# Kernel tuning notes

Measured on AMD Instinct MI355X. Metric: run time of the kernel, lower is better.

Reference implementation:

```python
import jax, jax.numpy as jnp
import numpy as np

T, S, B, H, L = 1024, 4096, 1, 1024, 2


def setup_inputs() -> dict:
    key = jax.random.key(0)
    ks = jax.random.split(key, 16)
    sc = 1.0 / np.sqrt(H)
    r = lambda k, shp: (jax.random.normal(k, shp, jnp.float32) * sc)
    return {
        'input_sequence': jax.random.normal(ks[0], (T, B, H), jnp.float32),
        'encoder_out': jax.random.normal(ks[1], (S, B, H), jnp.float32),
        'hidden_state': jax.random.normal(ks[2], (L, B, H), jnp.float32),
        'cell_state': jax.random.normal(ks[3], (L, B, H), jnp.float32),
        'w_ih0': r(ks[4], (4 * H, H)), 'w_hh0': r(ks[5], (4 * H, H)),
        'b_ih0': r(ks[6], (4 * H,)), 'b_hh0': r(ks[7], (4 * H,)),
        'w_ih1': r(ks[8], (4 * H, H)), 'w_hh1': r(ks[9], (4 * H, H)),
        'b_ih1': r(ks[10], (4 * H,)), 'b_hh1': r(ks[11], (4 * H,)),
        'w_cat': r(ks[12], (H, 2 * H)), 'b_cat': r(ks[13], (H,)),
    }


def _lstm_layer(x, h0, c0, w_ih, w_hh, bias):
    # x: [T, B, I]; precompute input projection once (torch gate order i,f,g,o)
    xg = jnp.einsum('tbi,gi->tbg', x, w_ih) + bias  # [T, B, 4H]

    def step(carry, xg_t):
        h, c = carry
        gates = xg_t + h @ w_hh.T
        i, f, g, o = jnp.split(gates, 4, axis=-1)
        c = jax.nn.sigmoid(f) * c + jax.nn.sigmoid(i) * jnp.tanh(g)
        h = jax.nn.sigmoid(o) * jnp.tanh(c)
        return (h, c), h

    (h, c), ys = jax.lax.scan(step, (h0, c0), xg)
    return ys, h, c  # ys: [T, B, H]


def reference(input_sequence, encoder_out, hidden_state, cell_state,
              w_ih0, w_hh0, b_ih0, b_hh0, w_ih1, w_hh1, b_ih1, b_hh1,
              w_cat, b_cat):
    out0, h1, c1 = _lstm_layer(input_sequence, hidden_state[0], cell_state[0],
                               w_ih0, w_hh0, b_ih0 + b_hh0)
    out1, h2, c2 = _lstm_layer(out0, hidden_state[1], cell_state[1],
                               w_ih1, w_hh1, b_ih1 + b_hh1)
    hN = jnp.stack([h1, h2])  # [L, B, H]
    cN = jnp.stack([c1, c2])

    # Attention ('dot'): scores_i = <enc_i, h_last>, softmax over source dim.
    enc = encoder_out[:, 0, :]        # [S, H] (batch = 1)
    target = h2[0]                     # [H]
    scores = enc @ target              # [S]  (replaces per-step torch.dot loop)
    weights = jax.nn.softmax(scores)   # [S]
    context = jnp.einsum('s,sh->h', weights, enc)  # [H] (replaces mul/reduce loop)

    cat = jnp.concatenate([context, h2[0]])          # [2H]
    attentional_hidden = jnp.tanh(cat @ w_cat.T + b_cat)[None, :]  # [1, H]
    return out1, (hN, cN), attentional_hidden
```

## Files before the change

### kernel.cpp

```cpp
#include <hip/hip_runtime.h>
#include <hip/hip_bf16.h>
#include <math.h>

#define T_STEPS 1024
#define HDIM    1024
#define SDIM    4096

__device__ __forceinline__ float sigmoid_f(float x) {
    return __builtin_amdgcn_rcpf(1.0f + __expf(-x));
}
__device__ __forceinline__ float tanh_f(float x) {
    return 1.0f - 2.0f * __builtin_amdgcn_rcpf(1.0f + __expf(2.0f * x));
}

union H2U { unsigned u; _Float16 h[2]; unsigned short s[2]; };

typedef _Float16 half2v __attribute__((ext_vector_type(2)));

__device__ __forceinline__ float fdot2_(unsigned w, unsigned h, float acc) {
#if __has_builtin(__builtin_amdgcn_fdot2)
    return __builtin_amdgcn_fdot2(__builtin_bit_cast(half2v, w),
                                  __builtin_bit_cast(half2v, h), acc, false);
#else
    const half2v a = __builtin_bit_cast(half2v, w);
    const half2v b = __builtin_bit_cast(half2v, h);
    return acc + (float)a[0] * (float)b[0] + (float)a[1] * (float)b[1];
#endif
}

#define GLOAD16(dst, p) asm volatile("global_load_dwordx4 %0, %1, off" \
                                     : "=v"(dst) : "v"(p))
#define GWAIT() asm volatile("s_waitcnt vmcnt(0)" ::: "memory")

__device__ __forceinline__ unsigned long long lda64(const unsigned long long* p) {
    return __hip_atomic_load(p, __ATOMIC_RELAXED, __HIP_MEMORY_SCOPE_AGENT);
}

__device__ __forceinline__ void poll2(const unsigned long long* p0,
                                      const unsigned long long* p1,
                                      unsigned long long& r0, unsigned long long& r1) {
    unsigned long long c0 = lda64(p0), c1 = lda64(p1);
    for (;;) {
        const unsigned long long n0 = lda64(p0);
        const unsigned long long n1 = lda64(p1);
        const unsigned t = (unsigned)c0 | (unsigned)(c0 >> 32) |
                           (unsigned)c1 | (unsigned)(c1 >> 32);
        if (t < 0xFFFF0000u) break;
        c0 = n0; c1 = n1;
    }
    r0 = c0; r1 = c1;
}

__device__ __forceinline__ unsigned pack_pair(unsigned long long v) {
    return (unsigned)(v & 0xFFFFu) | (((unsigned)(v >> 32) & 0xFFFFu) << 16);
}

__global__ __launch_bounds__(256) void cvt_fp16(
    const float* __restrict__ in, _Float16* __restrict__ o, int n)
{
    const int i = (blockIdx.x * 256 + threadIdx.x) * 8;
    if (i + 7 < n) {
        const float4 a = *(const float4*)(in + i);
        const float4 b = *(const float4*)(in + i + 4);
        H2U p0, p1, p2, p3;
        p0.h[0] = (_Float16)a.x; p0.h[1] = (_Float16)a.y;
        p1.h[0] = (_Float16)a.z; p1.h[1] = (_Float16)a.w;
        p2.h[0] = (_Float16)b.x; p2.h[1] = (_Float16)b.y;
        p3.h[0] = (_Float16)b.z; p3.h[1] = (_Float16)b.w;
        *(uint4*)(o + i) = make_uint4(p0.u, p1.u, p2.u, p3.u);
    }
}

__global__ __launch_bounds__(256) void bias_sum(
    const float* __restrict__ a, const float* __restrict__ b, float* __restrict__ o)
{
    const int i = blockIdx.x * 256 + threadIdx.x;
    o[i] = a[i] + b[i];
}

__global__ __launch_bounds__(256) void gemm_xg_h(
    const float* __restrict__ X, const float* __restrict__ W,
    const float* __restrict__ b1, const float* __restrict__ b2,
    _Float16* __restrict__ C, int M, int N, int K)
{
    __shared__ float As[16][64];
    __shared__ float Bs[16][64];
    const int tid = threadIdx.x;
    const int m0 = blockIdx.y * 64, n0 = blockIdx.x * 64;
    const int tx = tid & 15, ty = tid >> 4;
    const int lr = tid >> 2, ls = (tid & 3) << 2;
    float acc[4][4] = {};

    for (int kt = 0; kt < K; kt += 16) {
        const float4 xa = *(const float4*)(X + (size_t)(m0 + lr) * K + kt + ls);
        const float4 wb = *(const float4*)(W + (size_t)(n0 + lr) * K + kt + ls);
        __syncthreads();
        As[ls + 0][lr] = xa.x; As[ls + 1][lr] = xa.y; As[ls + 2][lr] = xa.z; As[ls + 3][lr] = xa.w;
        Bs[ls + 0][lr] = wb.x; Bs[ls + 1][lr] = wb.y; Bs[ls + 2][lr] = wb.z; Bs[ls + 3][lr] = wb.w;
        __syncthreads();
#pragma unroll
        for (int k = 0; k < 16; ++k) {
            const float4 a = *(const float4*)&As[k][ty << 2];
            const float4 b = *(const float4*)&Bs[k][tx << 2];
            acc[0][0] += a.x * b.x; acc[0][1] += a.x * b.y; acc[0][2] += a.x * b.z; acc[0][3] += a.x * b.w;
            acc[1][0] += a.y * b.x; acc[1][1] += a.y * b.y; acc[1][2] += a.y * b.z; acc[1][3] += a.y * b.w;
            acc[2][0] += a.z * b.x; acc[2][1] += a.z * b.y; acc[2][2] += a.z * b.z; acc[2][3] += a.z * b.w;
            acc[3][0] += a.w * b.x; acc[3][1] += a.w * b.y; acc[3][2] += a.w * b.z; acc[3][3] += a.w * b.w;
        }
    }
    const int gn = n0 + (tx << 2);
    const float4 bias = make_float4(b1[gn + 0] + b2[gn + 0], b1[gn + 1] + b2[gn + 1],
                                    b1[gn + 2] + b2[gn + 2], b1[gn + 3] + b2[gn + 3]);
#pragma unroll
    for (int i = 0; i < 4; ++i) {
        H2U q0, q1;
        q0.h[0] = (_Float16)(acc[i][0] + bias.x);
        q0.h[1] = (_Float16)(acc[i][1] + bias.y);
        q1.h[0] = (_Float16)(acc[i][2] + bias.z);
        q1.h[1] = (_Float16)(acc[i][3] + bias.w);
        *(uint2*)(C + (size_t)(m0 + (ty << 2) + i) * N + gn) = make_uint2(q0.u, q1.u);
    }
}

__global__ __launch_bounds__(256)
__attribute__((amdgpu_waves_per_eu(1, 1)))
void lstm_fused2(
    const _Float16* __restrict__ xg0h,
    const _Float16* __restrict__ wh0h,
    const _Float16* __restrict__ wi1h,
    const _Float16* __restrict__ wh1h,
    const float* __restrict__ b1s,
    const float* __restrict__ h0all, const float* __restrict__ c0all,
    float* __restrict__ out1,
    float* __restrict__ hN, float* __restrict__ cN,
    unsigned* bc0, unsigned* bc1)
{
    __shared__ unsigned hbuf2[512];
    __shared__ unsigned xbuf2[512];

    const int tid  = threadIdx.x;
    const int wave = tid >> 6, lane = tid & 63;
    const int w    = lane & 7;
    const int o    = (wave << 3) | (lane >> 3);
    const int col_local = o >> 2, gate = o & 3;
    const int layer = blockIdx.x >> 7;
    const int blk   = blockIdx.x & 127;
    const int col   = blk * 8 + col_local;
    const int r     = gate * HDIM + col;
    const int B     = lane & 32;

    float cst = c0all[layer * HDIM + col];
    float h_out = 0.0f;

    if (layer == 0) {
        const unsigned* wb = (const unsigned*)wh0h + (size_t)r * 512 + w * 64;
        uint4 wh[16];
#pragma unroll
        for (int i = 0; i < 16; ++i) GLOAD16(wh[i], (const void*)(wb + i * 4));
        GWAIT();

        for (int t = 0; t < T_STEPS; ++t) {
            const _Float16* xr = xg0h + (size_t)t * 4096 + col;
            const float xb0 = (float)xr[0],    xb1 = (float)xr[1024];
            const float xb2 = (float)xr[2048], xb3 = (float)xr[3072];

            if (t == 0) {
                H2U a, b;
                a.h[0] = (_Float16)h0all[2 * tid];
                a.h[1] = (_Float16)h0all[2 * tid + 1];
                b.h[0] = (_Float16)h0all[512 + 2 * tid];
                b.h[1] = (_Float16)h0all[512 + 2 * tid + 1];
                hbuf2[tid] = a.u; hbuf2[tid + 256] = b.u;
            } else {
                const unsigned long long* row = (const unsigned long long*)(bc0 + (size_t)(t - 1) * 1024);
                unsigned long long v0, v1;
                poll2(row + tid, row + tid + 256, v0, v1);
                hbuf2[tid] = pack_pair(v0); hbuf2[tid + 256] = pack_pair(v1);
            }
            __syncthreads();

            float acc = 0.f;
#pragma unroll
            for (int q = 0; q < 16; ++q) {
                const uint4 hv = *(const uint4*)&hbuf2[w * 64 + q * 4];
                acc = fdot2_(wh[q].x, hv.x, acc);
                acc = fdot2_(wh[q].y, hv.y, acc);
                acc = fdot2_(wh[q].z, hv.z, acc);
                acc = fdot2_(wh[q].w, hv.w, acc);
            }
            acc += __shfl_xor(acc, 1, 64);
            acc += __shfl_xor(acc, 2, 64);
            acc += __shfl_xor(acc, 4, 64);
            const float g0 = __shfl(acc, B + 0, 64);
            const float g1 = __shfl(acc, B + 8, 64);
            const float g2 = __shfl(acc, B + 16, 64);
            const float g3 = __shfl(acc, B + 24, 64);

            const float ig = sigmoid_f(g0 + xb0);
            const float fg = sigmoid_f(g1 + xb1);
            const float gv = tanh_f(g2 + xb2);
            const float oo = sigmoid_f(g3 + xb3);
            cst = fg * cst + ig * gv;
            h_out = oo * tanh_f(cst);

            if ((lane & 31) == 0) {
                H2U hv; hv.h[0] = (_Float16)h_out;
                __hip_atomic_store(bc0 + (size_t)t * 1024 + col, (unsigned)hv.s[0],
                                   __ATOMIC_RELAXED, __HIP_MEMORY_SCOPE_AGENT);
            }
        }
        if ((lane & 31) == 0) { hN[col] = h_out; cN[col] = cst; }
    } else {
        const unsigned* wxb = (const unsigned*)wi1h + (size_t)r * 512 + w * 64;
        const unsigned* whb = (const unsigned*)wh1h + (size_t)r * 512 + w * 64;
        uint4 wx[16], wh[16];
#pragma unroll
        for (int i = 0; i < 16; ++i) GLOAD16(wx[i], (const void*)(wxb + i * 4));
#pragma unroll
        for (int i = 0; i < 16; ++i) GLOAD16(wh[i], (const void*)(whb + i * 4));
        GWAIT();

        const float* br = b1s + col;
        const float xb0 = br[0],    xb1 = br[1024];
        const float xb2 = br[2048], xb3 = br[3072];

        for (int t = 0; t < T_STEPS; ++t) {
            if (t == 0) {
                H2U a, b;
                a.h[0] = (_Float16)h0all[HDIM + 2 * tid];
                a.h[1] = (_Float16)h0all[HDIM + 2 * tid + 1];
                b.h[0] = (_Float16)h0all[HDIM + 512 + 2 * tid];
                b.h[1] = (_Float16)h0all[HDIM + 512 + 2 * tid + 1];
                hbuf2[tid] = a.u; hbuf2[tid + 256] = b.u;
            }
            {
                const unsigned long long* row = (const unsigned long long*)(bc0 + (size_t)t * 1024);
                unsigned long long v0, v1;
                poll2(row + tid, row + tid + 256, v0, v1);
                xbuf2[tid] = pack_pair(v0); xbuf2[tid + 256] = pack_pair(v1);
            }
            __syncthreads();

            float acc = 0.f;
#pragma unroll
            for (int q = 0; q < 16; ++q) {
                const uint4 xv = *(const uint4*)&xbuf2[w * 64 + q * 4];
                acc = fdot2_(wx[q].x, xv.x, acc);
                acc = fdot2_(wx[q].y, xv.y, acc);
                acc = fdot2_(wx[q].z, xv.z, acc);
                acc = fdot2_(wx[q].w, xv.w, acc);
            }

            if (t > 0) {
                const unsigned long long* row = (const unsigned long long*)(bc1 + (size_t)(t - 1) * 1024);
                unsigned long long v0, v1;
                poll2(row + tid, row + tid + 256, v0, v1);
                hbuf2[tid] = pack_pair(v0); hbuf2[tid + 256] = pack_pair(v1);
            }
            __syncthreads();

#pragma unroll
            for (int q = 0; q < 16; ++q) {
                const uint4 hv = *(const uint4*)&hbuf2[w * 64 + q * 4];
                acc = fdot2_(wh[q].x, hv.x, acc);
                acc = fdot2_(wh[q].y, hv.y, acc);
                acc = fdot2_(wh[q].z, hv.z, acc);
                acc = fdot2_(wh[q].w, hv.w, acc);
            }
            acc += __shfl_xor(acc, 1, 64);
            acc += __shfl_xor(acc, 2, 64);
            acc += __shfl_xor(acc, 4, 64);
            const float g0 = __shfl(acc, B + 0, 64);
            const float g1 = __shfl(acc, B + 8, 64);
            const float g2 = __shfl(acc, B + 16, 64);
            const float g3 = __shfl(acc, B + 24, 64);

            const float ig = sigmoid_f(g0 + xb0);
            const float fg = sigmoid_f(g1 + xb1);
            const float gv = tanh_f(g2 + xb2);
            const float oo = sigmoid_f(g3 + xb3);
            cst = fg * cst + ig * gv;
            h_out = oo * tanh_f(cst);

            if ((lane & 31) == 0) {
                out1[(size_t)t * HDIM + col] = h_out;
                H2U hv; hv.h[0] = (_Float16)h_out;
                __hip_atomic_store(bc1 + (size_t)t * 1024 + col, (unsigned)hv.s[0],
                                   __ATOMIC_RELAXED, __HIP_MEMORY_SCOPE_AGENT);
            }
            __syncthreads();
        }
        if ((lane & 31) == 0) { hN[HDIM + col] = h_out; cN[HDIM + col] = cst; }
    }
}

__global__ __launch_bounds__(256) void attn_scores(
    const float* __restrict__ enc, const float* __restrict__ tgt,
    float* __restrict__ scores)
{
    const int lane = threadIdx.x & 63, wv = threadIdx.x >> 6;
    const int s = (blockIdx.x << 2) + wv;
    const float4* e4 = (const float4*)(enc + (size_t)s * HDIM);
    const float4* t4 = (const float4*)tgt;
    float acc = 0.f;
#pragma unroll
    for (int k = 0; k < 4; ++k) {
        const int idx = lane + (k << 6);
        const float4 e = e4[idx], t = t4[idx];
        acc += e.x * t.x + e.y * t.y + e.z * t.z + e.w * t.w;
    }
#pragma unroll
    for (int d = 32; d > 0; d >>= 1) acc += __shfl_xor(acc, d, 64);
    if (lane == 0) scores[s] = acc;
}

__global__ __launch_bounds__(1024) void attn_softmax(
    const float* __restrict__ scores, float* __restrict__ wts)
{
    __shared__ float rmax[16];
    __shared__ float rsum[16];
    const int tid = threadIdx.x, lane = tid & 63, wv = tid >> 6;
    const float4 v = ((const float4*)scores)[tid];
    float m = fmaxf(fmaxf(v.x, v.y), fmaxf(v.z, v.w));
#pragma unroll
    for (int d = 32; d > 0; d >>= 1) m = fmaxf(m, __shfl_xor(m, d, 64));
    if (lane == 0) rmax[wv] = m;
    __syncthreads();
    float gm = rmax[0];
#pragma unroll
    for (int i = 1; i < 16; ++i) gm = fmaxf(gm, rmax[i]);
    const float e0 = expf(v.x - gm), e1 = expf(v.y - gm), e2 = expf(v.z - gm), e3 = expf(v.w - gm);
    float s = e0 + e1 + e2 + e3;
#pragma unroll
    for (int d = 32; d > 0; d >>= 1) s += __shfl_xor(s, d, 64);
    if (lane == 0) rsum[wv] = s;
    __syncthreads();
    float gs = 0.f;
#pragma unroll
    for (int i = 0; i < 16; ++i) gs += rsum[i];
    const float inv = 1.0f / gs;
    ((float4*)wts)[tid] = make_float4(e0 * inv, e1 * inv, e2 * inv, e3 * inv);
}

__global__ __launch_bounds__(256) void attn_context(
    const float* __restrict__ wts, const float* __restrict__ enc,
    float* __restrict__ ctx)
{
    __shared__ float red[16][16];
    const int ci = threadIdx.x & 15, ri = threadIdx.x >> 4;
    const int col = blockIdx.x * 16 + ci;
    float acc = 0.f;
    for (int r = ri; r < SDIM; r += 16)
        acc += wts[r] * enc[(size_t)r * HDIM + col];
    red[ri][ci] = acc;
    __syncthreads();
    if (ri == 0) {
        float s = 0.f;
#pragma unroll
        for (int k = 0; k < 16; ++k) s += red[k][ci];
        ctx[col] = s;
    }
}

__global__ __launch_bounds__(256) void attn_final(
    const float* __restrict__ ctx, const float* __restrict__ h2,
    const float* __restrict__ w_cat, const float* __restrict__ b_cat,
    float* __restrict__ out)
{
    const int lane = threadIdx.x & 63, wv = threadIdx.x >> 6;
    const int j = (blockIdx.x << 2) + wv;
    const float4* wc1 = (const float4*)(w_cat + (size_t)j * 2048);
    const float4* wc2 = (const float4*)(w_cat + (size_t)j * 2048 + 1024);
    const float4* c4 = (const float4*)ctx;
    const float4* h4 = (const float4*)h2;
    float acc = 0.f;
#pragma unroll
    for (int k = 0; k < 4; ++k) {
        const int idx = lane + (k << 6);
        float4 a = wc1[idx], b = c4[idx];
        acc += a.x * b.x + a.y * b.y + a.z * b.z + a.w * b.w;
        a = wc2[idx]; b = h4[idx];
        acc += a.x * b.x + a.y * b.y + a.z * b.z + a.w * b.w;
    }
#pragma unroll
    for (int d = 32; d > 0; d >>= 1) acc += __shfl_xor(acc, d, 64);
    if (lane == 0) out[j] = tanhf(acc + b_cat[j]);
}

extern "C" void kernel_launch(void* const* d_in, const int* in_sizes, int n_in,
                              void* d_out, int out_size, void* d_ws, size_t ws_size,
                              hipStream_t stream)
{
    (void)in_sizes; (void)n_in; (void)out_size; (void)ws_size;
    const float* x     = (const float*)d_in[0];
    const float* enc   = (const float*)d_in[1];
    const float* h0all = (const float*)d_in[2];
    const float* c0all = (const float*)d_in[3];
    const float* w_ih0 = (const float*)d_in[4];
    const float* w_hh0 = (const float*)d_in[5];
    const float* b_ih0 = (const float*)d_in[6];
    const float* b_hh0 = (const float*)d_in[7];
    const float* w_ih1 = (const float*)d_in[8];
    const float* w_hh1 = (const float*)d_in[9];
    const float* b_ih1 = (const float*)d_in[10];
    const float* b_hh1 = (const float*)d_in[11];
    const float* w_cat = (const float*)d_in[12];
    const float* b_cat = (const float*)d_in[13];
    float* out = (float*)d_out;

    float* out1 = out;
    float* hN   = out + 1048576;
    float* cN   = out + 1050624;
    float* attn = out + 1052672;

    char* wsb = (char*)d_ws;
    _Float16* xg0h = (_Float16*)(wsb);
    _Float16* wh0h = (_Float16*)(wsb + 8388608);
    _Float16* wi1h = (_Float16*)(wsb + 16777216);
    _Float16* wh1h = (_Float16*)(wsb + 25165824);
    float*    b1s  = (float*)   (wsb + 33554432);
    unsigned* bc0  = (unsigned*)(wsb + 33570816);
    unsigned* bc1  = (unsigned*)(wsb + 37765120);
    float* scores  = (float*)   (wsb + 41959424);
    float* wts     = (float*)   (wsb + 41975808);
    float* ctx     = (float*)   (wsb + 41992192);

    hipMemsetAsync(bc0, 0xFF, 2 * 4194304, stream);
    cvt_fp16<<<2048, 256, 0, stream>>>(w_hh0, wh0h, 4194304);
    cvt_fp16<<<2048, 256, 0, stream>>>(w_ih1, wi1h, 4194304);
    cvt_fp16<<<2048, 256, 0, stream>>>(w_hh1, wh1h, 4194304);
    bias_sum<<<16, 256, 0, stream>>>(b_ih1, b_hh1, b1s);

    dim3 gg(64, 16);
    gemm_xg_h<<<gg, 256, 0, stream>>>(x, w_ih0, b_ih0, b_hh0, xg0h, 1024, 4096, 1024);
    lstm_fused2<<<256, 256, 0, stream>>>(xg0h, wh0h, wi1h, wh1h, b1s,
                                         h0all, c0all, out1, hN, cN, bc0, bc1);
    attn_scores<<<1024, 256, 0, stream>>>(enc, hN + 1024, scores);
    attn_softmax<<<1, 1024, 0, stream>>>(scores, wts);
    attn_context<<<64, 256, 0, stream>>>(wts, enc, ctx);
    attn_final<<<256, 256, 0, stream>>>(ctx, hN + 1024, w_cat, b_cat, attn);
}
```

Measured before the change: 3.470 ms.

## Merge layer-1 polls and barriers, double-buffer shared vectors, pad LDS rows

In the layer-1 branch, the input-vector poll and the recurrent-state poll are combined into one four-address spin, and the two projections are computed in a single loop after one barrier. The shared x/h buffers are double-buffered by step parity, which allows the trailing per-step barrier to be dropped. Shared-memory rows are padded by four words every 64 to reduce bank conflicts on the strided uint4 reads. The aim is to cut one to two barriers and one serialized poll from each recurrent step. The cost is that the x projection no longer overlaps the wait on h.

```diff
diff --git a/kernel.cpp b/kernel.cpp
--- a/kernel.cpp
+++ b/kernel.cpp
@@ -43,17 +43,41 @@
     for (;;) {
         const unsigned long long n0 = lda64(p0);
         const unsigned long long n1 = lda64(p1);
-        const unsigned t = (unsigned)c0 | (unsigned)(c0 >> 32) |
+        const unsigned m = (unsigned)c0 | (unsigned)(c0 >> 32) |
                            (unsigned)c1 | (unsigned)(c1 >> 32);
-        if (t < 0xFFFF0000u) break;
+        if (m < 0xFFFF0000u) break;
         c0 = n0; c1 = n1;
     }
     r0 = c0; r1 = c1;
+}
+
+__device__ __forceinline__ void poll4(const unsigned long long* p0,
+                                      const unsigned long long* p1,
+                                      const unsigned long long* p2,
+                                      const unsigned long long* p3,
+                                      unsigned long long& r0, unsigned long long& r1,
+                                      unsigned long long& r2, unsigned long long& r3) {
+    unsigned long long c0 = lda64(p0), c1 = lda64(p1), c2 = lda64(p2), c3 = lda64(p3);
+    for (;;) {
+        const unsigned long long n0 = lda64(p0);
+        const unsigned long long n1 = lda64(p1);
+        const unsigned long long n2 = lda64(p2);
+        const unsigned long long n3 = lda64(p3);
+        const unsigned m = (unsigned)c0 | (unsigned)(c0 >> 32) |
+                           (unsigned)c1 | (unsigned)(c1 >> 32) |
+                           (unsigned)c2 | (unsigned)(c2 >> 32) |
+                           (unsigned)c3 | (unsigned)(c3 >> 32);
+        if (m < 0xFFFF0000u) break;
+        c0 = n0; c1 = n1; c2 = n2; c3 = n3;
+    }
+    r0 = c0; r1 = c1; r2 = c2; r3 = c3;
 }
 
 __device__ __forceinline__ unsigned pack_pair(unsigned long long v) {
     return (unsigned)(v & 0xFFFFu) | (((unsigned)(v >> 32) & 0xFFFFu) << 16);
 }
+
+#define HPAD(i) ((i) + (((i) >> 6) << 2))
 
 __global__ __launch_bounds__(256) void cvt_fp16(
     const float* __restrict__ in, _Float16* __restrict__ o, int n)
@@ -124,7 +148,7 @@
 
 __global__ __launch_bounds__(256)
 __attribute__((amdgpu_waves_per_eu(1, 1)))
-void lstm_fused2(
+void lstm_fused3(
     const _Float16* __restrict__ xg0h,
     const _Float16* __restrict__ wh0h,
     const _Float16* __restrict__ wi1h,
@@ -135,9 +159,7 @@
     float* __restrict__ hN, float* __restrict__ cN,
     unsigned* bc0, unsigned* bc1)
 {
-    __shared__ unsigned hbuf2[512];
-    __shared__ unsigned xbuf2[512];
-
+    __shared__ unsigned smem[2176];
     const int tid  = threadIdx.x;
     const int wave = tid >> 6, lane = tid & 63;
     const int w    = lane & 7;
@@ -159,6 +181,7 @@
         for (int i = 0; i < 16; ++i) GLOAD16(wh[i], (const void*)(wb + i * 4));
         GWAIT();
 
+        unsigned* hb = smem;
         for (int t = 0; t < T_STEPS; ++t) {
             const _Float16* xr = xg0h + (size_t)t * 4096 + col;
             const float xb0 = (float)xr[0],    xb1 = (float)xr[1024];
@@ -170,19 +193,20 @@
                 a.h[1] = (_Float16)h0all[2 * tid + 1];
                 b.h[0] = (_Float16)h0all[512 + 2 * tid];
                 b.h[1] = (_Float16)h0all[512 + 2 * tid + 1];
-                hbuf2[tid] = a.u; hbuf2[tid + 256] = b.u;
+                hb[HPAD(tid)] = a.u; hb[HPAD(tid + 256)] = b.u;
             } else {
                 const unsigned long long* row = (const unsigned long long*)(bc0 + (size_t)(t - 1) * 1024);
                 unsigned long long v0, v1;
                 poll2(row + tid, row + tid + 256, v0, v1);
-                hbuf2[tid] = pack_pair(v0); hbuf2[tid + 256] = pack_pair(v1);
+                hb[HPAD(tid)] = pack_pair(v0); hb[HPAD(tid + 256)] = pack_pair(v1);
             }
             __syncthreads();
 
+            const unsigned* hw = hb + w * 68;
             float acc = 0.f;
 #pragma unroll
             for (int q = 0; q < 16; ++q) {
-                const uint4 hv = *(const uint4*)&hbuf2[w * 64 + q * 4];
+                const uint4 hv = *(const uint4*)&hw[q * 4];
                 acc = fdot2_(wh[q].x, hv.x, acc);
                 acc = fdot2_(wh[q].y, hv.y, acc);
                 acc = fdot2_(wh[q].z, hv.z, acc);
@@ -225,43 +249,42 @@
         const float xb2 = br[2048], xb3 = br[3072];
 
         for (int t = 0; t < T_STEPS; ++t) {
+            unsigned* xbc = smem + (t & 1) * 544;
+            unsigned* hbc = smem + 1088 + (t & 1) * 544;
+
             if (t == 0) {
+                const unsigned long long* rx = (const unsigned long long*)(bc0);
+                unsigned long long v0, v1;
+                poll2(rx + tid, rx + tid + 256, v0, v1);
+                xbc[HPAD(tid)] = pack_pair(v0); xbc[HPAD(tid + 256)] = pack_pair(v1);
                 H2U a, b;
                 a.h[0] = (_Float16)h0all[HDIM + 2 * tid];
                 a.h[1] = (_Float16)h0all[HDIM + 2 * tid + 1];
                 b.h[0] = (_Float16)h0all[HDIM + 512 + 2 * tid];
                 b.h[1] = (_Float16)h0all[HDIM + 512 + 2 * tid + 1];
-                hbuf2[tid] = a.u; hbuf2[tid + 256] = b.u;
-            }
-            {
-                const unsigned long long* row = (const unsigned long long*)(bc0 + (size_t)t * 1024);
-                unsigned long long v0, v1;
-                poll2(row + tid, row + tid + 256, v0, v1);
-                xbuf2[tid] = pack_pair(v0); xbuf2[tid + 256] = pack_pair(v1);
+                hbc[HPAD(tid)] = a.u; hbc[HPAD(tid + 256)] = b.u;
+            } else {
+                const unsigned long long* rx = (const unsigned long long*)(bc0 + (size_t)t * 1024);
+                const unsigned long long* rh = (const unsigned long long*)(bc1 + (size_t)(t - 1) * 1024);
+                unsigned long long vx0, vx1, vh0, vh1;
+                poll4(rx + tid, rx + tid + 256, rh + tid, rh + tid + 256,
+                      vx0, vx1, vh0, vh1);
+                xbc[HPAD(tid)] = pack_pair(vx0); xbc[HPAD(tid + 256)] = pack_pair(vx1);
+                hbc[HPAD(tid)] = pack_pair(vh0); hbc[HPAD(tid + 256)] = pack_pair(vh1);
             }
             __syncthreads();
 
+            const unsigned* xw = xbc + w * 68;
+            const unsigned* hw = hbc + w * 68;
             float acc = 0.f;
 #pragma unroll
             for (int q = 0; q < 16; ++q) {
-                const uint4 xv = *(const uint4*)&xbuf2[w * 64 + q * 4];
+                const uint4 xv = *(const uint4*)&xw[q * 4];
+                const uint4 hv = *(const uint4*)&hw[q * 4];
                 acc = fdot2_(wx[q].x, xv.x, acc);
                 acc = fdot2_(wx[q].y, xv.y, acc);
                 acc = fdot2_(wx[q].z, xv.z, acc);
                 acc = fdot2_(wx[q].w, xv.w, acc);
-            }
-
-            if (t > 0) {
-                const unsigned long long* row = (const unsigned long long*)(bc1 + (size_t)(t - 1) * 1024);
-                unsigned long long v0, v1;
-                poll2(row + tid, row + tid + 256, v0, v1);
-                hbuf2[tid] = pack_pair(v0); hbuf2[tid + 256] = pack_pair(v1);
-            }
-            __syncthreads();
-
-#pragma unroll
-            for (int q = 0; q < 16; ++q) {
-                const uint4 hv = *(const uint4*)&hbuf2[w * 64 + q * 4];
                 acc = fdot2_(wh[q].x, hv.x, acc);
                 acc = fdot2_(wh[q].y, hv.y, acc);
                 acc = fdot2_(wh[q].z, hv.z, acc);
@@ -288,7 +311,6 @@
                 __hip_atomic_store(bc1 + (size_t)t * 1024 + col, (unsigned)hv.s[0],
                                    __ATOMIC_RELAXED, __HIP_MEMORY_SCOPE_AGENT);
             }
-            __syncthreads();
         }
         if ((lane & 31) == 0) { hN[HDIM + col] = h_out; cN[HDIM + col] = cst; }
     }
@@ -433,7 +455,7 @@
 
     dim3 gg(64, 16);
     gemm_xg_h<<<gg, 256, 0, stream>>>(x, w_ih0, b_ih0, b_hh0, xg0h, 1024, 4096, 1024);
-    lstm_fused2<<<256, 256, 0, stream>>>(xg0h, wh0h, wi1h, wh1h, b1s,
+    lstm_fused3<<<256, 256, 0, stream>>>(xg0h, wh0h, wi1h, wh1h, b1s,
                                          h0all, c0all, out1, hN, cN, bc0, bc1);
     attn_scores<<<1024, 256, 0, stream>>>(enc, hN + 1024, scores);
     attn_softmax<<<1, 1024, 0, stream>>>(scores, wts);
```

Result: slower. 3.635 ms (+4.8%).
